# Optimization experiments

Hardware: AMD Instinct MI355X
Metric: run time of the kernel (lower is better)

The kernel has to match this reference:

```python
import jax, jax.numpy as jnp
import numpy as np

H, W = 256, 832
B = 2
SEARCH_W, SEARCH_H = 7, 3
SPARSITY_RAD = 2
SENSE_RANGE = 10
PIX_W = 20.0          # pixel_distance_weight
ALPHA_W = 0.7         # alpha_distance_weight
MULLINE_W = 15.0      # pixel_mulline_distance_weight
ALPHA_PAD = 0.6       # alpha_padding
INF = 1e9


def _sorted_offsets(span_x, span_y):
    xs, ys = np.meshgrid(span_x, span_y)
    xs = xs.flatten(); ys = ys.flatten()
    order = np.argsort(xs ** 2 + ys ** 2, kind='stable')
    return xs[order].astype(np.int32), ys[order].astype(np.int32)


def setup_inputs() -> dict:
    key = jax.random.key(0)
    k1, k2 = jax.random.split(key)
    src = (jax.random.uniform(k1, (B, 1, H, W)) < 0.02).astype(jnp.float32)
    dst = (jax.random.uniform(k2, (B, 1, H, W)) < 0.02).astype(jnp.float32)
    xx, yy = _sorted_offsets(np.arange(-SEARCH_W, SEARCH_W + 1), np.arange(-SEARCH_H, SEARCH_H + 1))
    sxs, sys_ = np.meshgrid(np.arange(-SPARSITY_RAD, SPARSITY_RAD + 1), np.arange(-SPARSITY_RAD, SPARSITY_RAD + 1))
    sxx = sxs.flatten().astype(np.int32); syy = sys_.flatten().astype(np.int32)
    cxx, cyy = _sorted_offsets(np.arange(-SENSE_RANGE, SENSE_RANGE + 1), np.arange(-SENSE_RANGE, SENSE_RANGE + 1))
    return {"binMapsrc": src, "binMapdst": dst,
            "xx": jnp.asarray(xx), "yy": jnp.asarray(yy),
            "sxx": jnp.asarray(sxx), "syy": jnp.asarray(syy),
            "cxx": jnp.asarray(cxx), "cyy": jnp.asarray(cyy)}


def _orientation(m):
    # local edge orientation from a 3x3 box-blurred map
    b = sum(jnp.roll(jnp.roll(m, di, 0), dj, 1) for di in (-1, 0, 1) for dj in (-1, 0, 1))
    gy, gx = jnp.gradient(b)
    return jnp.arctan2(gy, gx)


def _morph_single(src, dst, xx, yy, sxx, syy, cxx, cyy):
    gy, gx = jnp.meshgrid(jnp.arange(H, dtype=jnp.int32), jnp.arange(W, dtype=jnp.int32), indexing='ij')

    def gather(offy, offx, arr, fill):
        ii = gy[None] + offy[:, None, None]          # [K,H,W]
        jj = gx[None] + offx[:, None, None]
        inb = (ii >= 0) & (ii < H) & (jj >= 0) & (jj < W)
        vals = arr[jnp.clip(ii, 0, H - 1), jnp.clip(jj, 0, W - 1)]
        return jnp.where(inb, vals, fill)

    src_e = src > 0.5
    # --- sparsify source edge points: keep min-linear-index edge in each sparsity window ---
    lin = jnp.where(src_e, (gy * W + gx).astype(jnp.float32), INF)
    keep = src_e & (lin == gather(syy, sxx, lin, INF).min(0))
    # --- windowed correspondence search with distance + orientation scoring ---
    theta_s = _orientation(src)
    theta_d = _orientation(dst)
    hit = gather(yy, xx, dst, 0.0) > 0.5             # [K,H,W]
    ang = 1.0 - jnp.cos(theta_s[None] - gather(yy, xx, theta_d, 0.0))
    dist = jnp.sqrt((xx * xx + yy * yy).astype(jnp.float32))
    score = jnp.where(hit, PIX_W * dist[:, None, None] + MULLINE_W * ALPHA_W * ang, INF)
    kbest = jnp.argmin(score, axis=0)                # [H,W]
    active = keep & (score.min(0) < 0.5 * INF)
    dispx = jnp.where(active, xx[kbest].astype(jnp.float32), 0.0)
    dispy = jnp.where(active, yy[kbest].astype(jnp.float32), 0.0)
    # --- diffuse sparse displacements over the sense window (scan keeps memory small) ---
    R = SENSE_RANGE
    pad = lambda a: jnp.pad(a, ((R, R), (R, R)))
    pdx, pdy, pm = pad(dispx), pad(dispy), pad(active.astype(jnp.float32))
    wk = jnp.exp(-jnp.sqrt((cxx * cxx + cyy * cyy).astype(jnp.float32)) / (0.5 * R))

    def body(carry, inp):
        nx, ny, den = carry
        dy_, dx_, w = inp
        sl = lambda a: jax.lax.dynamic_slice(a, (R + dy_, R + dx_), (H, W))
        return (nx + w * sl(pdx), ny + w * sl(pdy), den + w * sl(pm)), None

    zeros = jnp.zeros((H, W), jnp.float32)
    (nx, ny, den), _ = jax.lax.scan(body, (zeros, zeros, zeros), (cyy, cxx, wk))
    mdx = ALPHA_PAD * nx / (den + 1e-6)
    mdy = ALPHA_PAD * ny / (den + 1e-6)
    morphedx = gx.astype(jnp.float32) + mdx
    morphedy = gy.astype(jnp.float32) + mdy
    return jnp.stack([morphedx, morphedy], 0)        # [2,H,W]


def reference(binMapsrc, binMapdst, xx, yy, sxx, syy, cxx, cyy):
    f = lambda s, d: _morph_single(s, d, xx, yy, sxx, syy, cxx, cyy)
    return jax.vmap(f)(binMapsrc[:, 0], binMapdst[:, 0])  # [B,2,H,W]
```

## Files before the change

kernel.cpp:

```cpp
#include <hip/hip_runtime.h>
#include <math.h>

#define BB 2
#define HH 256
#define WW 832
#define HWIMG (HH * WW)

#define TS 16
#define TXN (WW / TS)
#define TYN (HH / TS)
#define KCAP 160

#define SRH 40
#define SRW 40
#define DRH 46
#define DRW 56

__device__ inline float theta_at(const float* __restrict__ m, int i, int j) {
    int ri[5], cj[5];
#pragma unroll
    for (int t = 0; t < 5; ++t) {
        int r = i + t - 2; r = (r < 0) ? r + HH : (r >= HH ? r - HH : r);
        int c = j + t - 2; c = (c < 0) ? c + WW : (c >= WW ? c - WW : c);
        ri[t] = r * WW; cj[t] = c;
    }
    float S[5][5];
#pragma unroll
    for (int a = 0; a < 5; ++a)
#pragma unroll
        for (int c = 0; c < 5; ++c)
            S[a][c] = m[ri[a] + cj[c]];
    float ct[5], cm[5], cb[5];
#pragma unroll
    for (int c = 0; c < 5; ++c) {
        ct[c] = S[0][c] + S[1][c] + S[2][c];
        cm[c] = S[1][c] + S[2][c] + S[3][c];
        cb[c] = S[2][c] + S[3][c] + S[4][c];
    }
    float Bm = ct[1] + ct[2] + ct[3];
    float Bp = cb[1] + cb[2] + cb[3];
    float Bl = cm[0] + cm[1] + cm[2];
    float Br = cm[2] + cm[3] + cm[4];
    float Bc = cm[1] + cm[2] + cm[3];
    float gy = (i == 0) ? (Bp - Bc) : (i == HH - 1) ? (Bc - Bm) : 0.5f * (Bp - Bm);
    float gx = (j == 0) ? (Br - Bc) : (j == WW - 1) ? (Bc - Bl) : 0.5f * (Br - Bl);
    return atan2f(gy, gx);
}

__device__ inline float theta_lds(const float* __restrict__ m, int stride,
                                  int li, int lj) {
    const float* p = m + (li - 2) * stride + (lj - 2);
    float S[5][5];
#pragma unroll
    for (int a = 0; a < 5; ++a)
#pragma unroll
        for (int c = 0; c < 5; ++c)
            S[a][c] = p[a * stride + c];
    float ct[5], cm[5], cb[5];
#pragma unroll
    for (int c = 0; c < 5; ++c) {
        ct[c] = S[0][c] + S[1][c] + S[2][c];
        cm[c] = S[1][c] + S[2][c] + S[3][c];
        cb[c] = S[2][c] + S[3][c] + S[4][c];
    }
    float Bm = ct[1] + ct[2] + ct[3];
    float Bp = cb[1] + cb[2] + cb[3];
    float Bl = cm[0] + cm[1] + cm[2];
    float Br = cm[2] + cm[3] + cm[4];
    float gy = 0.5f * (Bp - Bm);
    float gx = 0.5f * (Br - Bl);
    return atan2f(gy, gx);
}

__global__ __launch_bounds__(256) void fused_kernel(
        const float* __restrict__ src, const float* __restrict__ dst,
        const int* __restrict__ xx, const int* __restrict__ yy, int K,
        float* __restrict__ out) {
    __shared__ float slds[SRH * SRW];
    __shared__ float dlds[DRH * DRW];
    __shared__ int kox[128], koy[128];
    __shared__ float kd[128];
    __shared__ int recs[KCAP];
    __shared__ float tss[KCAP];
    __shared__ float4 ent[KCAP];
    __shared__ float wt[441];
    __shared__ int nkeep, ne;

    int tid = threadIdx.x;
    int b = blockIdx.z;
    int i0 = blockIdx.y * TS;
    int j0 = blockIdx.x * TS;
    const float* sb = src + b * HWIMG;
    const float* db = dst + b * HWIMG;

    if (tid == 0) { nkeep = 0; ne = 0; }

    for (int t = tid; t < SRH * SRW; t += 256) {
        int r = i0 - 12 + t / SRW, c = j0 - 12 + t % SRW;
        int cr = min(max(r, 0), HH - 1), cc = min(max(c, 0), WW - 1);
        float v = sb[cr * WW + cc];
        slds[t] = (r >= 0 && r < HH && c >= 0 && c < WW) ? v : 0.f;
    }
    for (int t = tid; t < DRH * DRW; t += 256) {
        int r = i0 - 15 + t / DRW, c = j0 - 20 + t % DRW;
        int cr = min(max(r, 0), HH - 1), cc = min(max(c, 0), WW - 1);
        float v = db[cr * WW + cc];
        dlds[t] = (r >= 0 && r < HH && c >= 0 && c < WW) ? v : 0.f;
    }
    for (int t = tid; t < K; t += 256) {
        int ox = xx[t], oy = yy[t];
        kox[t] = ox; koy[t] = oy;
        kd[t] = 20.0f * sqrtf((float)(ox * ox + oy * oy));
    }
    for (int t = tid; t < 441; t += 256) {
        int dy = t / 21 - 10;
        int dx = t % 21 - 10;
        wt[t] = expf(-sqrtf((float)(dx * dx + dy * dy)) / 5.0f);
    }
    __syncthreads();

    for (int t = tid; t < 36 * 36; t += 256) {
        int rl = t / 36, cl = t % 36;
        int li = rl + 2, lj = cl + 2;
        if (slds[li * SRW + lj] > 0.5f) {
            float m = 0.f;
#pragma unroll
            for (int p = 0; p < 12; ++p) {
                int di = (p < 5) ? -2 : (p < 10 ? -1 : 0);
                int dj = (p < 5) ? (p - 2) : (p < 10 ? (p - 7) : (p - 12));
                m = fmaxf(m, slds[(li + di) * SRW + (lj + dj)]);
            }
            if (m <= 0.5f) {
                int gi = i0 - 10 + rl, gj = j0 - 10 + cl;
                bool inner = (gi >= 2) && (gi < HH - 2) && (gj >= 2) && (gj < WW - 2);
                float ts = inner ? theta_lds(slds, SRW, li, lj)
                                 : theta_at(sb, gi, gj);
                int pos = atomicAdd(&nkeep, 1);
                if (pos < KCAP) { recs[pos] = gj | (gi << 10); tss[pos] = ts; }
            }
        }
    }
    __syncthreads();

    int nk = (nkeep < KCAP) ? nkeep : KCAP;
    int lane = tid & 63;
    int wv = tid >> 6;
    for (int w = wv; w < nk; w += 4) {
        int rec = recs[w];
        int kj = rec & 1023;
        int ki = rec >> 10;
        float ts = tss[w];
        int kli = ki - i0 + 15;
        int klj = kj - j0 + 20;

        float best = 1e9f;
        int bk = 1 << 20;
#pragma unroll
        for (int rr = 0; rr < 2; ++rr) {
            int k = lane + rr * 64;
            if (k < K) {
                int pli = kli + koy[k], plj = klj + kox[k];
                if (dlds[pli * DRW + plj] > 0.5f) {
                    int pi = ki + koy[k], pj = kj + kox[k];
                    bool inner = (pi >= 2) && (pi < HH - 2) && (pj >= 2) && (pj < WW - 2);
                    float td = inner ? theta_lds(dlds, DRW, pli, plj)
                                     : theta_at(db, pi, pj);
                    float sc = kd[k] + 10.5f * (1.0f - cosf(ts - td));
                    if (sc < best || (sc == best && k < bk)) { best = sc; bk = k; }
                }
            }
        }
#pragma unroll
        for (int off = 32; off >= 1; off >>= 1) {
            float ob = __shfl_down(best, off, 64);
            int ok = __shfl_down(bk, off, 64);
            if (ob < best || (ob == best && ok < bk)) { best = ob; bk = ok; }
        }
        if (lane == 0 && best < 5e8f) {
            int pos = atomicAdd(&ne, 1);
            if (pos < KCAP)
                ent[pos] = make_float4((float)kj, (float)ki,
                                       (float)kox[bk], (float)koy[bk]);
        }
    }
    __syncthreads();

    int nn = (ne < KCAP) ? ne : KCAP;
    int gj = j0 + (tid & 15);
    int gi = i0 + (tid >> 4);
    float nx = 0.f, ny = 0.f, de = 0.f;
    for (int c = 0; c < nn; ++c) {
        float4 E = ent[c];
        int dj = (int)E.x - gj;
        int di = (int)E.y - gi;
        if (dj >= -10 && dj <= 10 && di >= -10 && di <= 10) {
            float w = wt[(di + 10) * 21 + dj + 10];
            de += w; nx += w * E.z; ny += w * E.w;
        }
    }
    float inv = 0.6f / (de + 1e-6f);
    int obase = b * 2 * HWIMG;
    out[obase + gi * WW + gj] = (float)gj + nx * inv;
    out[obase + HWIMG + gi * WW + gj] = (float)gi + ny * inv;
}

extern "C" void kernel_launch(void* const* d_in, const int* in_sizes, int n_in,
                              void* d_out, int out_size, void* d_ws, size_t ws_size,
                              hipStream_t stream) {
    const float* src = (const float*)d_in[0];
    const float* dst = (const float*)d_in[1];
    const int* xx = (const int*)d_in[2];
    const int* yy = (const int*)d_in[3];
    int K = in_sizes[2];

    float* out = (float*)d_out;
    dim3 grid(TXN, TYN, BB);
    fused_kernel<<<grid, dim3(256), 0, stream>>>(src, dst, xx, yy, K, out);
}
```

Before: 108.8 us.

## Compact edges and candidate hits into work lists, replace wave reductions with atomicMin

Loads the source and destination halos with row-per-wave coalesced loops into tiles padded to 64 columns. Edge pixels are first compacted into a list, so the sparsify test only runs on actual edges. Destination candidate hits are compacted into a second list, and orientation and score are computed only for those hits. The best candidate per kept point is then chosen with a packed 64-bit atomicMin instead of a per-wave shuffle reduction. This trades extra barriers and fixed list caps (ECAP, HCAP), which can drop edges or hits if exceeded, for better lane utilisation on the sparse maps.

```diff
diff --git a/kernel.cpp b/kernel.cpp
--- a/kernel.cpp
+++ b/kernel.cpp
@@ -9,12 +9,15 @@
 #define TS 16
 #define TXN (WW / TS)
 #define TYN (HH / TS)
+
 #define KCAP 160
+#define ECAP 128
+#define HCAP 192
 
 #define SRH 40
-#define SRW 40
+#define SRW 64
 #define DRH 46
-#define DRW 56
+#define DRW 64
 
 __device__ inline float theta_at(const float* __restrict__ m, int i, int j) {
     int ri[5], cj[5];
@@ -78,124 +81,156 @@
         float* __restrict__ out) {
     __shared__ float slds[SRH * SRW];
     __shared__ float dlds[DRH * DRW];
-    __shared__ int kox[128], koy[128];
-    __shared__ float kd[128];
+    __shared__ int kox[112], koy[112];
+    __shared__ float kd[112];
+    __shared__ float wt[441];
+    __shared__ int elist[ECAP];
     __shared__ int recs[KCAP];
     __shared__ float tss[KCAP];
+    __shared__ unsigned long long best64[KCAP];
+    __shared__ int hits[HCAP];
     __shared__ float4 ent[KCAP];
-    __shared__ float wt[441];
-    __shared__ int nkeep, ne;
+    __shared__ int nedge, nkeep, nhit;
 
     int tid = threadIdx.x;
+    int lane = tid & 63;
+    int wv = tid >> 6;
     int b = blockIdx.z;
     int i0 = blockIdx.y * TS;
     int j0 = blockIdx.x * TS;
     const float* sb = src + b * HWIMG;
     const float* db = dst + b * HWIMG;
 
-    if (tid == 0) { nkeep = 0; ne = 0; }
-
-    for (int t = tid; t < SRH * SRW; t += 256) {
-        int r = i0 - 12 + t / SRW, c = j0 - 12 + t % SRW;
-        int cr = min(max(r, 0), HH - 1), cc = min(max(c, 0), WW - 1);
-        float v = sb[cr * WW + cc];
-        slds[t] = (r >= 0 && r < HH && c >= 0 && c < WW) ? v : 0.f;
-    }
-    for (int t = tid; t < DRH * DRW; t += 256) {
-        int r = i0 - 15 + t / DRW, c = j0 - 20 + t % DRW;
-        int cr = min(max(r, 0), HH - 1), cc = min(max(c, 0), WW - 1);
-        float v = db[cr * WW + cc];
-        dlds[t] = (r >= 0 && r < HH && c >= 0 && c < WW) ? v : 0.f;
+    if (tid == 0) { nedge = 0; nkeep = 0; nhit = 0; }
+    for (int t = tid; t < KCAP; t += 256) best64[t] = ~0ULL;
+
+    {
+        int c = j0 - 12 + lane;
+        int cc = min(max(c, 0), WW - 1);
+        bool cok = (c >= 0) && (c < WW);
+#pragma unroll
+        for (int rr = 0; rr < 10; ++rr) {
+            int row = wv + 4 * rr;
+            int r = i0 - 12 + row;
+            int cr = min(max(r, 0), HH - 1);
+            float v = sb[cr * WW + cc];
+            slds[row * SRW + lane] = (cok && r >= 0 && r < HH) ? v : 0.f;
+        }
+    }
+    {
+        int c = j0 - 20 + lane;
+        int cc = min(max(c, 0), WW - 1);
+        bool cok = (c >= 0) && (c < WW);
+#pragma unroll
+        for (int rr = 0; rr < 12; ++rr) {
+            int row = wv + 4 * rr;
+            if (row < DRH) {
+                int r = i0 - 15 + row;
+                int cr = min(max(r, 0), HH - 1);
+                float v = db[cr * WW + cc];
+                dlds[row * DRW + lane] = (cok && r >= 0 && r < HH) ? v : 0.f;
+            }
+        }
     }
     for (int t = tid; t < K; t += 256) {
         int ox = xx[t], oy = yy[t];
         kox[t] = ox; koy[t] = oy;
         kd[t] = 20.0f * sqrtf((float)(ox * ox + oy * oy));
     }
-    for (int t = tid; t < 441; t += 256) {
-        int dy = t / 21 - 10;
-        int dx = t % 21 - 10;
-        wt[t] = expf(-sqrtf((float)(dx * dx + dy * dy)) / 5.0f);
-    }
-    __syncthreads();
-
-    for (int t = tid; t < 36 * 36; t += 256) {
-        int rl = t / 36, cl = t % 36;
+    for (int t = tid; t < 21 * 32; t += 256) {
+        int dy = t >> 5, dx = t & 31;
+        if (dx < 21)
+            wt[dy * 21 + dx] = expf(-sqrtf((float)((dx - 10) * (dx - 10) +
+                                                   (dy - 10) * (dy - 10))) / 5.0f);
+    }
+    __syncthreads();
+
+    for (int t = tid; t < 36 * 64; t += 256) {
+        int cl = t & 63, rl = t >> 6;
+        if (cl < 36 && slds[(rl + 2) * SRW + (cl + 2)] > 0.5f) {
+            int p = atomicAdd(&nedge, 1);
+            if (p < ECAP) elist[p] = (rl << 8) | cl;
+        }
+    }
+    __syncthreads();
+
+    int nE = (nedge < ECAP) ? nedge : ECAP;
+    for (int t = tid; t < nE; t += 256) {
+        int rl = elist[t] >> 8, cl = elist[t] & 255;
         int li = rl + 2, lj = cl + 2;
-        if (slds[li * SRW + lj] > 0.5f) {
-            float m = 0.f;
-#pragma unroll
-            for (int p = 0; p < 12; ++p) {
-                int di = (p < 5) ? -2 : (p < 10 ? -1 : 0);
-                int dj = (p < 5) ? (p - 2) : (p < 10 ? (p - 7) : (p - 12));
-                m = fmaxf(m, slds[(li + di) * SRW + (lj + dj)]);
+        float m = 0.f;
+#pragma unroll
+        for (int p = 0; p < 12; ++p) {
+            int di = (p < 5) ? -2 : (p < 10 ? -1 : 0);
+            int dj = (p < 5) ? (p - 2) : (p < 10 ? (p - 7) : (p - 12));
+            m = fmaxf(m, slds[(li + di) * SRW + (lj + dj)]);
+        }
+        if (m <= 0.5f) {
+            int gi = i0 - 10 + rl, gj = j0 - 10 + cl;
+            bool inner = (gi >= 2) && (gi < HH - 2) && (gj >= 2) && (gj < WW - 2);
+            float ts = inner ? theta_lds(slds, SRW, li, lj)
+                             : theta_at(sb, gi, gj);
+            int p = atomicAdd(&nkeep, 1);
+            if (p < KCAP) { recs[p] = gj | (gi << 10); tss[p] = ts; }
+        }
+    }
+    __syncthreads();
+
+    int nk = (nkeep < KCAP) ? nkeep : KCAP;
+    for (int t = tid; t < nk * 128; t += 256) {
+        int w = t >> 7, k = t & 127;
+        if (k < K) {
+            int rec = recs[w];
+            int kj = rec & 1023, ki = rec >> 10;
+            int pli = ki - i0 + 15 + koy[k];
+            int plj = kj - j0 + 20 + kox[k];
+            if (dlds[pli * DRW + plj] > 0.5f) {
+                int p = atomicAdd(&nhit, 1);
+                if (p < HCAP) hits[p] = (w << 7) | k;
             }
-            if (m <= 0.5f) {
-                int gi = i0 - 10 + rl, gj = j0 - 10 + cl;
-                bool inner = (gi >= 2) && (gi < HH - 2) && (gj >= 2) && (gj < WW - 2);
-                float ts = inner ? theta_lds(slds, SRW, li, lj)
-                                 : theta_at(sb, gi, gj);
-                int pos = atomicAdd(&nkeep, 1);
-                if (pos < KCAP) { recs[pos] = gj | (gi << 10); tss[pos] = ts; }
-            }
-        }
-    }
-    __syncthreads();
-
-    int nk = (nkeep < KCAP) ? nkeep : KCAP;
-    int lane = tid & 63;
-    int wv = tid >> 6;
-    for (int w = wv; w < nk; w += 4) {
+        }
+    }
+    __syncthreads();
+
+    int nh = (nhit < HCAP) ? nhit : HCAP;
+    for (int t = tid; t < nh; t += 256) {
+        int w = hits[t] >> 7, k = hits[t] & 127;
         int rec = recs[w];
-        int kj = rec & 1023;
-        int ki = rec >> 10;
-        float ts = tss[w];
-        int kli = ki - i0 + 15;
-        int klj = kj - j0 + 20;
-
-        float best = 1e9f;
-        int bk = 1 << 20;
-#pragma unroll
-        for (int rr = 0; rr < 2; ++rr) {
-            int k = lane + rr * 64;
-            if (k < K) {
-                int pli = kli + koy[k], plj = klj + kox[k];
-                if (dlds[pli * DRW + plj] > 0.5f) {
-                    int pi = ki + koy[k], pj = kj + kox[k];
-                    bool inner = (pi >= 2) && (pi < HH - 2) && (pj >= 2) && (pj < WW - 2);
-                    float td = inner ? theta_lds(dlds, DRW, pli, plj)
-                                     : theta_at(db, pi, pj);
-                    float sc = kd[k] + 10.5f * (1.0f - cosf(ts - td));
-                    if (sc < best || (sc == best && k < bk)) { best = sc; bk = k; }
-                }
-            }
-        }
-#pragma unroll
-        for (int off = 32; off >= 1; off >>= 1) {
-            float ob = __shfl_down(best, off, 64);
-            int ok = __shfl_down(bk, off, 64);
-            if (ob < best || (ob == best && ok < bk)) { best = ob; bk = ok; }
-        }
-        if (lane == 0 && best < 5e8f) {
-            int pos = atomicAdd(&ne, 1);
-            if (pos < KCAP)
-                ent[pos] = make_float4((float)kj, (float)ki,
-                                       (float)kox[bk], (float)koy[bk]);
-        }
-    }
-    __syncthreads();
-
-    int nn = (ne < KCAP) ? ne : KCAP;
+        int kj = rec & 1023, ki = rec >> 10;
+        int pi = ki + koy[k], pj = kj + kox[k];
+        bool inner = (pi >= 2) && (pi < HH - 2) && (pj >= 2) && (pj < WW - 2);
+        float td = inner ? theta_lds(dlds, DRW, pi - i0 + 15, pj - j0 + 20)
+                         : theta_at(db, pi, pj);
+        float sc = kd[k] + 10.5f * (1.0f - cosf(tss[w] - td));
+        unsigned long long pk =
+            ((unsigned long long)__float_as_uint(sc) << 32) | (unsigned)k;
+        atomicMin(&best64[w], pk);
+    }
+    __syncthreads();
+
+    for (int t = tid; t < nk; t += 256) {
+        unsigned long long v = best64[t];
+        if (v != ~0ULL) {
+            int k = (int)(v & 0xffffffffULL);
+            int rec = recs[t];
+            ent[t] = make_float4((float)(rec & 1023), (float)(rec >> 10),
+                                 (float)kox[k], (float)koy[k]);
+        } else {
+            ent[t] = make_float4(-1e4f, -1e4f, 0.f, 0.f);
+        }
+    }
+    __syncthreads();
+
     int gj = j0 + (tid & 15);
     int gi = i0 + (tid >> 4);
     float nx = 0.f, ny = 0.f, de = 0.f;
-    for (int c = 0; c < nn; ++c) {
-        float4 E = ent[c];
+    for (int w = 0; w < nk; ++w) {
+        float4 E = ent[w];
         int dj = (int)E.x - gj;
         int di = (int)E.y - gi;
         if (dj >= -10 && dj <= 10 && di >= -10 && di <= 10) {
-            float w = wt[(di + 10) * 21 + dj + 10];
-            de += w; nx += w * E.z; ny += w * E.w;
+            float w_ = wt[(di + 10) * 21 + dj + 10];
+            de += w_; nx += w_ * E.z; ny += w_ * E.w;
         }
     }
     float inv = 0.6f / (de + 1e-6f);
```

Result: faster. 91.68 us (-15.8%).
